# Performance work log

Hardware: AMD Instinct MI355X
Metric: run time of the kernel (lower is better)

## Reference

```python
import jax, jax.numpy as jnp
import numpy as np

EPS = 1e-8
TWO_PI = 2.0 * np.pi


def diff_round(x):
    # differentiable soft-round used for mask sharpening
    return x - jnp.sin(TWO_PI * x) / TWO_PI


def setup_inputs() -> dict:
    key = jax.random.key(0)
    k1, k2 = jax.random.split(key)
    B, N, P, Q = 8, 16384, 8, 8  # batch, superpixel areas, patch h, patch w
    sv_area_image = jax.random.normal(k1, (B, N, P, Q), dtype=jnp.float32)
    sv_area_mask = jax.random.uniform(k2, (B, N, P, Q), dtype=jnp.float32)
    return {"sv_area_image": sv_area_image, "sv_area_mask": sv_area_mask}


def reference(sv_area_image, sv_area_mask):
    # reshaped_mask = diff_round(diff_round(mask)) as in get_area_loss
    m = diff_round(diff_round(sv_area_mask))
    # per-area masked mean / variance (get_single_area_loss, doubly vmapped)
    masked = sv_area_image * m                      # [B, N, P, Q]
    msum = jnp.sum(m, axis=(-2, -1)) + EPS          # [B, N]
    mean = jnp.sum(masked, axis=(-2, -1)) / msum    # [B, N]
    dev = (masked - mean[..., None, None]) * m      # [B, N, P, Q]
    varr = jnp.sum(dev * dev, axis=(-2, -1)) / msum # [B, N]
    return jnp.mean(varr)
```

## Files before the change

kernel.cpp:

```cpp
#include <hip/hip_runtime.h>

#define TPB 256

__device__ __forceinline__ float sin2pi(float x) {
    return __builtin_amdgcn_sinf(x);
}

__device__ __forceinline__ float diff_round(float x) {
    return __builtin_fmaf(sin2pi(x), -0.15915494309189533577f, x);
}

template <int CTRL>
__device__ __forceinline__ float dpp_add(float v) {
    int i = __float_as_int(v);
    int m = __builtin_amdgcn_update_dpp(i, i, CTRL, 0xF, 0xF, false);
    return v + __int_as_float(m);
}

__device__ __forceinline__ float row_sum16(float s) {
    s = dpp_add<0xB1>(s);
    s = dpp_add<0x4E>(s);
    s = dpp_add<0x124>(s);
    s = dpp_add<0x128>(s);
    return s;
}

__global__ __launch_bounds__(TPB) void area_var_partial(
    const float* __restrict__ img, const float* __restrict__ msk,
    float* __restrict__ partial, int ntiles) {
    const int tid  = threadIdx.x;
    const int wave = tid >> 6;
    const int lane = tid & 63;
    const int grp  = lane >> 4;
    const int j    = lane & 15;

    float acc = 0.0f;
    const int tiles_per_block = (TPB / 64) * 4;
    for (int tbase = blockIdx.x * tiles_per_block; tbase < ntiles;
         tbase += gridDim.x * tiles_per_block) {
        const int tile = tbase + wave * 4 + grp;
        float4 iv = make_float4(0.f, 0.f, 0.f, 0.f);
        float4 mv = make_float4(0.f, 0.f, 0.f, 0.f);
        if (tile < ntiles) {
            const size_t off = (size_t)tile * 64 + (size_t)j * 4;
            iv = *reinterpret_cast<const float4*>(img + off);
            mv = *reinterpret_cast<const float4*>(msk + off);
        }
        float m0 = diff_round(diff_round(mv.x));
        float m1 = diff_round(diff_round(mv.y));
        float m2 = diff_round(diff_round(mv.z));
        float m3 = diff_round(diff_round(mv.w));
        float x0 = iv.x * m0, x1 = iv.y * m1, x2 = iv.z * m2, x3 = iv.w * m3;

        float sm = row_sum16((m0 + m1) + (m2 + m3));
        float sx = row_sum16((x0 + x1) + (x2 + x3));
        const float inv_msum = __builtin_amdgcn_rcpf(sm + 1e-8f);
        const float mean = sx * inv_msum;

        float d0 = (x0 - mean) * m0;
        float d1 = (x1 - mean) * m1;
        float d2 = (x2 - mean) * m2;
        float d3 = (x3 - mean) * m3;
        float sd = row_sum16((d0 * d0 + d1 * d1) + (d2 * d2 + d3 * d3));

        acc += sd * inv_msum;
    }
    acc += __shfl_xor(acc, 16, 64);
    acc += __shfl_xor(acc, 32, 64);

    __shared__ float wsum[TPB / 64];
    if (lane == 0) wsum[wave] = acc;
    __syncthreads();
    if (tid == 0) partial[blockIdx.x] = (wsum[0] + wsum[1]) + (wsum[2] + wsum[3]);
}

__global__ __launch_bounds__(TPB) void final_reduce(
    const float* __restrict__ partial, float* __restrict__ out,
    int n, float inv_count) {
    float s = 0.f;
    for (int i = threadIdx.x; i < n; i += TPB) s += partial[i];
    #pragma unroll
    for (int d = 1; d < 64; d <<= 1) s += __shfl_xor(s, d, 64);
    __shared__ float wsum[TPB / 64];
    const int wave = threadIdx.x >> 6;
    const int lane = threadIdx.x & 63;
    if (lane == 0) wsum[wave] = s;
    __syncthreads();
    if (threadIdx.x == 0)
        out[0] = ((wsum[0] + wsum[1]) + (wsum[2] + wsum[3])) * inv_count;
}

extern "C" void kernel_launch(void* const* d_in, const int* in_sizes, int n_in,
                              void* d_out, int out_size, void* d_ws, size_t ws_size,
                              hipStream_t stream) {
    const float* img = (const float*)d_in[0];
    const float* msk = (const float*)d_in[1];
    float* out = (float*)d_out;
    float* partial = (float*)d_ws;

    const int ntiles = in_sizes[0] / 64;
    int nblocks = (ntiles + 15) / 16;
    if (nblocks > 2048) nblocks = 2048;

    area_var_partial<<<nblocks, TPB, 0, stream>>>(img, msk, partial, ntiles);
    final_reduce<<<1, TPB, 0, stream>>>(partial, out, nblocks,
                                        1.0f / (float)ntiles);
}
```

Measured before the change: 94.77 us.

## Fuse final reduction into main kernel via last-block atomic counter

Replaces the two-kernel partial-then-final reduction with a single kernel in which each block writes its partial sum, bumps an atomic counter, and the last block to finish performs the final reduction. An async memset resets the counter before each launch. The main loop also gets an unroll-by-2 hint. This removes the second kernel's launch gap but adds a memset node and fence/atomic overhead per block.

After: 146.0 us. 1.54x slower.

```diff
diff --git a/kernel.cpp b/kernel.cpp
--- a/kernel.cpp
+++ b/kernel.cpp
@@ -1,6 +1,7 @@
 #include <hip/hip_runtime.h>
 
 #define TPB 256
+#define MAX_BLOCKS 2048
 
 __device__ __forceinline__ float sin2pi(float x) {
     return __builtin_amdgcn_sinf(x);
@@ -25,9 +26,10 @@
     return s;
 }
 
-__global__ __launch_bounds__(TPB) void area_var_partial(
+__global__ __launch_bounds__(TPB) void area_var_fused(
     const float* __restrict__ img, const float* __restrict__ msk,
-    float* __restrict__ partial, int ntiles) {
+    float* __restrict__ ws, float* __restrict__ out,
+    int ntiles, float inv_count) {
     const int tid  = threadIdx.x;
     const int wave = tid >> 6;
     const int lane = tid & 63;
@@ -36,6 +38,7 @@
 
     float acc = 0.0f;
     const int tiles_per_block = (TPB / 64) * 4;
+    #pragma unroll 2
     for (int tbase = blockIdx.x * tiles_per_block; tbase < ntiles;
          tbase += gridDim.x * tiles_per_block) {
         const int tile = tbase + wave * 4 + grp;
@@ -69,24 +72,28 @@
     acc += __shfl_xor(acc, 32, 64);
 
     __shared__ float wsum[TPB / 64];
+    __shared__ bool is_last;
     if (lane == 0) wsum[wave] = acc;
     __syncthreads();
-    if (tid == 0) partial[blockIdx.x] = (wsum[0] + wsum[1]) + (wsum[2] + wsum[3]);
-}
 
-__global__ __launch_bounds__(TPB) void final_reduce(
-    const float* __restrict__ partial, float* __restrict__ out,
-    int n, float inv_count) {
+    float* partial = ws + 16;
+    if (tid == 0) {
+        partial[blockIdx.x] = (wsum[0] + wsum[1]) + (wsum[2] + wsum[3]);
+        __threadfence();
+        unsigned old = atomicAdd(reinterpret_cast<unsigned*>(ws), 1u);
+        is_last = (old == gridDim.x - 1);
+    }
+    __syncthreads();
+    if (!is_last) return;
+
+    __threadfence();
     float s = 0.f;
-    for (int i = threadIdx.x; i < n; i += TPB) s += partial[i];
+    for (int i = tid; i < (int)gridDim.x; i += TPB) s += partial[i];
     #pragma unroll
     for (int d = 1; d < 64; d <<= 1) s += __shfl_xor(s, d, 64);
-    __shared__ float wsum[TPB / 64];
-    const int wave = threadIdx.x >> 6;
-    const int lane = threadIdx.x & 63;
     if (lane == 0) wsum[wave] = s;
     __syncthreads();
-    if (threadIdx.x == 0)
+    if (tid == 0)
         out[0] = ((wsum[0] + wsum[1]) + (wsum[2] + wsum[3])) * inv_count;
 }
 
@@ -96,13 +103,13 @@
     const float* img = (const float*)d_in[0];
     const float* msk = (const float*)d_in[1];
     float* out = (float*)d_out;
-    float* partial = (float*)d_ws;
+    float* ws  = (float*)d_ws;
 
     const int ntiles = in_sizes[0] / 64;
     int nblocks = (ntiles + 15) / 16;
-    if (nblocks > 2048) nblocks = 2048;
+    if (nblocks > MAX_BLOCKS) nblocks = MAX_BLOCKS;
 
-    area_var_partial<<<nblocks, TPB, 0, stream>>>(img, msk, partial, ntiles);
-    final_reduce<<<1, TPB, 0, stream>>>(partial, out, nblocks,
-                                        1.0f / (float)ntiles);
+    hipMemsetAsync(d_ws, 0, sizeof(unsigned), stream);
+    area_var_fused<<<nblocks, TPB, 0, stream>>>(img, msk, ws, out, ntiles,
+                                                1.0f / (float)ntiles);
 }
```

## Process two tiles per group and prefetch next iteration's loads

Applied to the files above, without the earlier changes.

Each 16-lane group now handles two adjacent tiles per iteration, and the loads for the next grid-stride iteration are issued before computing the current pair, giving software pipelining with more memory requests in flight. The block count is computed with 32 tiles per block but stays capped at 2048. This raises register use (four extra float4 prefetch buffers) and may lower occupancy in exchange for better latency hiding on a bandwidth-bound kernel.

Result: no change. 93.64 us (-1.2%).

```diff
diff --git a/kernel.cpp b/kernel.cpp
--- a/kernel.cpp
+++ b/kernel.cpp
@@ -1,6 +1,7 @@
 #include <hip/hip_runtime.h>
 
 #define TPB 256
+#define MAX_BLOCKS 2048
 
 __device__ __forceinline__ float sin2pi(float x) {
     return __builtin_amdgcn_sinf(x);
@@ -25,6 +26,43 @@
     return s;
 }
 
+__device__ __forceinline__ float tile_varr(const float4 iv, const float4 mv) {
+    float m0 = diff_round(diff_round(mv.x));
+    float m1 = diff_round(diff_round(mv.y));
+    float m2 = diff_round(diff_round(mv.z));
+    float m3 = diff_round(diff_round(mv.w));
+    float x0 = iv.x * m0, x1 = iv.y * m1, x2 = iv.z * m2, x3 = iv.w * m3;
+
+    float sm = row_sum16((m0 + m1) + (m2 + m3));
+    float sx = row_sum16((x0 + x1) + (x2 + x3));
+    const float inv_msum = __builtin_amdgcn_rcpf(sm + 1e-8f);
+    const float mean = sx * inv_msum;
+
+    float d0 = (x0 - mean) * m0;
+    float d1 = (x1 - mean) * m1;
+    float d2 = (x2 - mean) * m2;
+    float d3 = (x3 - mean) * m3;
+    float sd = row_sum16((d0 * d0 + d1 * d1) + (d2 * d2 + d3 * d3));
+    return sd * inv_msum;
+}
+
+__device__ __forceinline__ void load_pair(const float* __restrict__ img,
+                                          const float* __restrict__ msk,
+                                          int t0, int ntiles, int j,
+                                          float4& ivA, float4& mvA,
+                                          float4& ivB, float4& mvB) {
+    ivA = mvA = ivB = mvB = make_float4(0.f, 0.f, 0.f, 0.f);
+    const size_t off = (size_t)t0 * 64 + (size_t)j * 4;
+    if (t0 < ntiles) {
+        ivA = *reinterpret_cast<const float4*>(img + off);
+        mvA = *reinterpret_cast<const float4*>(msk + off);
+    }
+    if (t0 + 1 < ntiles) {
+        ivB = *reinterpret_cast<const float4*>(img + off + 64);
+        mvB = *reinterpret_cast<const float4*>(msk + off + 64);
+    }
+}
+
 __global__ __launch_bounds__(TPB) void area_var_partial(
     const float* __restrict__ img, const float* __restrict__ msk,
     float* __restrict__ partial, int ntiles) {
@@ -34,36 +72,26 @@
     const int grp  = lane >> 4;
     const int j    = lane & 15;
 
+    const int tiles_per_block = (TPB / 64) * 4 * 2;
+    const int stride = gridDim.x * tiles_per_block;
+    int t0 = blockIdx.x * tiles_per_block + (wave * 4 + grp) * 2;
+
     float acc = 0.0f;
-    const int tiles_per_block = (TPB / 64) * 4;
-    for (int tbase = blockIdx.x * tiles_per_block; tbase < ntiles;
-         tbase += gridDim.x * tiles_per_block) {
-        const int tile = tbase + wave * 4 + grp;
-        float4 iv = make_float4(0.f, 0.f, 0.f, 0.f);
-        float4 mv = make_float4(0.f, 0.f, 0.f, 0.f);
-        if (tile < ntiles) {
-            const size_t off = (size_t)tile * 64 + (size_t)j * 4;
-            iv = *reinterpret_cast<const float4*>(img + off);
-            mv = *reinterpret_cast<const float4*>(msk + off);
+    if (t0 < ntiles) {
+        float4 ivA, mvA, ivB, mvB;
+        load_pair(img, msk, t0, ntiles, j, ivA, mvA, ivB, mvB);
+        for (;;) {
+            const int nt = t0 + stride;
+            const bool more = nt < ntiles;
+            float4 nivA, nmvA, nivB, nmvB;
+            nivA = nmvA = nivB = nmvB = make_float4(0.f, 0.f, 0.f, 0.f);
+            if (more)
+                load_pair(img, msk, nt, ntiles, j, nivA, nmvA, nivB, nmvB);
+            acc += tile_varr(ivA, mvA);
+            acc += tile_varr(ivB, mvB);
+            if (!more) break;
+            ivA = nivA; mvA = nmvA; ivB = nivB; mvB = nmvB; t0 = nt;
         }
-        float m0 = diff_round(diff_round(mv.x));
-        float m1 = diff_round(diff_round(mv.y));
-        float m2 = diff_round(diff_round(mv.z));
-        float m3 = diff_round(diff_round(mv.w));
-        float x0 = iv.x * m0, x1 = iv.y * m1, x2 = iv.z * m2, x3 = iv.w * m3;
-
-        float sm = row_sum16((m0 + m1) + (m2 + m3));
-        float sx = row_sum16((x0 + x1) + (x2 + x3));
-        const float inv_msum = __builtin_amdgcn_rcpf(sm + 1e-8f);
-        const float mean = sx * inv_msum;
-
-        float d0 = (x0 - mean) * m0;
-        float d1 = (x1 - mean) * m1;
-        float d2 = (x2 - mean) * m2;
-        float d3 = (x3 - mean) * m3;
-        float sd = row_sum16((d0 * d0 + d1 * d1) + (d2 * d2 + d3 * d3));
-
-        acc += sd * inv_msum;
     }
     acc += __shfl_xor(acc, 16, 64);
     acc += __shfl_xor(acc, 32, 64);
@@ -99,8 +127,8 @@
     float* partial = (float*)d_ws;
 
     const int ntiles = in_sizes[0] / 64;
-    int nblocks = (ntiles + 15) / 16;
-    if (nblocks > 2048) nblocks = 2048;
+    int nblocks = (ntiles + 31) / 32;
+    if (nblocks > MAX_BLOCKS) nblocks = MAX_BLOCKS;
 
     area_var_partial<<<nblocks, TPB, 0, stream>>>(img, msk, partial, ntiles);
     final_reduce<<<1, TPB, 0, stream>>>(partial, out, nblocks,
```

## Process four tiles per 16-lane group with all loads issued upfront

Applied to the files above, without the earlier changes.

Replaces the grid-stride loop with a fixed mapping in which each 16-lane group handles four consecutive 8x8 tiles. All eight float4 loads are issued before any compute, which raises memory-level parallelism. The grid is sized to cover all tiles exactly, giving 2048 blocks of 64 tiles for this shape. Register use per thread goes up, and each group now reads four separate tiles with a stride of 256 bytes per lane row rather than interleaved tiles.

Result: no change. 94.00 us (-0.8%).

```diff
diff --git a/kernel.cpp b/kernel.cpp
--- a/kernel.cpp
+++ b/kernel.cpp
@@ -25,7 +25,27 @@
     return s;
 }
 
-__global__ __launch_bounds__(TPB) void area_var_partial(
+__device__ __forceinline__ float tile_varr(const float4 iv, const float4 mv) {
+    float m0 = diff_round(diff_round(mv.x));
+    float m1 = diff_round(diff_round(mv.y));
+    float m2 = diff_round(diff_round(mv.z));
+    float m3 = diff_round(diff_round(mv.w));
+    float x0 = iv.x * m0, x1 = iv.y * m1, x2 = iv.z * m2, x3 = iv.w * m3;
+
+    float sm = row_sum16((m0 + m1) + (m2 + m3));
+    float sx = row_sum16((x0 + x1) + (x2 + x3));
+    const float inv_msum = __builtin_amdgcn_rcpf(sm + 1e-8f);
+    const float mean = sx * inv_msum;
+
+    float d0 = (x0 - mean) * m0;
+    float d1 = (x1 - mean) * m1;
+    float d2 = (x2 - mean) * m2;
+    float d3 = (x3 - mean) * m3;
+    float sd = row_sum16((d0 * d0 + d1 * d1) + (d2 * d2 + d3 * d3));
+    return sd * inv_msum;
+}
+
+__global__ __launch_bounds__(TPB) void area_var4(
     const float* __restrict__ img, const float* __restrict__ msk,
     float* __restrict__ partial, int ntiles) {
     const int tid  = threadIdx.x;
@@ -34,37 +54,25 @@
     const int grp  = lane >> 4;
     const int j    = lane & 15;
 
-    float acc = 0.0f;
-    const int tiles_per_block = (TPB / 64) * 4;
-    for (int tbase = blockIdx.x * tiles_per_block; tbase < ntiles;
-         tbase += gridDim.x * tiles_per_block) {
-        const int tile = tbase + wave * 4 + grp;
-        float4 iv = make_float4(0.f, 0.f, 0.f, 0.f);
-        float4 mv = make_float4(0.f, 0.f, 0.f, 0.f);
-        if (tile < ntiles) {
-            const size_t off = (size_t)tile * 64 + (size_t)j * 4;
-            iv = *reinterpret_cast<const float4*>(img + off);
-            mv = *reinterpret_cast<const float4*>(msk + off);
+    const int t0 = blockIdx.x * 64 + (wave * 4 + grp) * 4;
+
+    float4 iv[4], mv[4];
+    #pragma unroll
+    for (int k = 0; k < 4; ++k) {
+        iv[k] = make_float4(0.f, 0.f, 0.f, 0.f);
+        mv[k] = make_float4(0.f, 0.f, 0.f, 0.f);
+        if (t0 + k < ntiles) {
+            const size_t off = (size_t)(t0 + k) * 64 + (size_t)j * 4;
+            iv[k] = *reinterpret_cast<const float4*>(img + off);
+            mv[k] = *reinterpret_cast<const float4*>(msk + off);
         }
-        float m0 = diff_round(diff_round(mv.x));
-        float m1 = diff_round(diff_round(mv.y));
-        float m2 = diff_round(diff_round(mv.z));
-        float m3 = diff_round(diff_round(mv.w));
-        float x0 = iv.x * m0, x1 = iv.y * m1, x2 = iv.z * m2, x3 = iv.w * m3;
+    }
 
-        float sm = row_sum16((m0 + m1) + (m2 + m3));
-        float sx = row_sum16((x0 + x1) + (x2 + x3));
-        const float inv_msum = __builtin_amdgcn_rcpf(sm + 1e-8f);
-        const float mean = sx * inv_msum;
+    float acc = tile_varr(iv[0], mv[0]);
+    acc += tile_varr(iv[1], mv[1]);
+    acc += tile_varr(iv[2], mv[2]);
+    acc += tile_varr(iv[3], mv[3]);
 
-        float d0 = (x0 - mean) * m0;
-        float d1 = (x1 - mean) * m1;
-        float d2 = (x2 - mean) * m2;
-        float d3 = (x3 - mean) * m3;
-        float sd = row_sum16((d0 * d0 + d1 * d1) + (d2 * d2 + d3 * d3));
-
-        acc += sd * inv_msum;
-    }
     acc += __shfl_xor(acc, 16, 64);
     acc += __shfl_xor(acc, 32, 64);
 
@@ -99,10 +107,9 @@
     float* partial = (float*)d_ws;
 
     const int ntiles = in_sizes[0] / 64;
-    int nblocks = (ntiles + 15) / 16;
-    if (nblocks > 2048) nblocks = 2048;
+    const int nblocks = (ntiles + 63) / 64;
 
-    area_var_partial<<<nblocks, TPB, 0, stream>>>(img, msk, partial, ntiles);
+    area_var4<<<nblocks, TPB, 0, stream>>>(img, msk, partial, ntiles);
     final_reduce<<<1, TPB, 0, stream>>>(partial, out, nblocks,
                                         1.0f / (float)ntiles);
 }
```
